# Performance work log

Hardware: AMD Instinct MI355X
Metric: run time of the kernel (lower is better)

## Reference

```python
import jax, jax.numpy as jnp
import numpy as np

EPS = 1e-05
IN_FEATURES = 1024
OUT_FEATURES = 512
M = 65536


def setup_inputs() -> dict:
    key = jax.random.key(0)
    k_x, k_w, k_b = jax.random.split(key, 3)
    x = jax.random.normal(k_x, (M, IN_FEATURES), dtype=jnp.float32)
    # kaiming_uniform(a=sqrt(5)) on [out, in]: bound = sqrt(6/((1+a^2)*fan_in)) = 1/sqrt(fan_in)
    bound = 1.0 / np.sqrt(IN_FEATURES)
    weight = jax.random.uniform(k_w, (OUT_FEATURES, IN_FEATURES), dtype=jnp.float32,
                                minval=-bound, maxval=bound)
    bias = jax.random.uniform(k_b, (OUT_FEATURES,), dtype=jnp.float32,
                              minval=-bound, maxval=bound)
    gamma = jnp.ones((OUT_FEATURES,), dtype=jnp.float32)
    beta = jnp.zeros((OUT_FEATURES,), dtype=jnp.float32)
    scale = jnp.ones((1,), dtype=jnp.float32)
    return {"x": x, "weight": weight, "bias": bias,
            "gamma": gamma, "beta": beta, "scale": scale}


def reference(x, weight, bias, gamma, beta, scale):
    # GEMM + bias: [M, N]
    acc = jnp.einsum('mk,nk->mn', x, weight) + bias[None, :]
    # Row-wise normalization over N (as the fused kernel computes per row)
    mean = jnp.mean(acc, axis=1, keepdims=True)
    var = jnp.mean((acc - mean) ** 2, axis=1, keepdims=True)
    normalized = (acc - mean) / jnp.sqrt(var + EPS)
    scaled = (normalized * gamma[None, :] + beta[None, :]) * scale[0]
    # Row softmax over N
    return jax.nn.softmax(scaled, axis=1)
```

## Files before the change

### kernel.cpp

```cpp
#include <hip/hip_runtime.h>
#include <hip/hip_bf16.h>

constexpr int KD = 1024;
constexpr int ND = 512;
constexpr int NT = 16;
constexpr float EPSV = 1e-5f;

using f32x4  = __attribute__((ext_vector_type(4))) float;
using bf16x8 = __attribute__((ext_vector_type(8))) short;
using u16x8  = __attribute__((ext_vector_type(8))) unsigned short;

__device__ __forceinline__ unsigned short f2bf(float f) {
  unsigned int u = __builtin_bit_cast(unsigned int, f);
  return (unsigned short)((u + 0x7fffu + ((u >> 16) & 1u)) >> 16);
}

__device__ __forceinline__ u16x8 pack8(float4 a, float4 b) {
  u16x8 v;
  v[0] = f2bf(a.x); v[1] = f2bf(a.y); v[2] = f2bf(a.z); v[3] = f2bf(a.w);
  v[4] = f2bf(b.x); v[5] = f2bf(b.y); v[6] = f2bf(b.z); v[7] = f2bf(b.w);
  return v;
}

__device__ __forceinline__ unsigned short cvt1(float f) {
  __hip_bfloat16 h = __float2bfloat16(f);
  return __builtin_bit_cast(unsigned short, h);
}

__device__ __forceinline__ void gload16(const void* g, void* l) {
  __builtin_amdgcn_global_load_lds(
      (const __attribute__((address_space(1))) void*)g,
      (__attribute__((address_space(3))) void*)l, 16, 0, 0);
}

#define WAITV4()  asm volatile("s_waitcnt vmcnt(4)" ::: "memory")
#define WAITV0()  asm volatile("s_waitcnt vmcnt(0)" ::: "memory")
#define LGKM0()   do { asm volatile("s_waitcnt lgkmcnt(0)" ::: "memory"); \
                       __builtin_amdgcn_sched_barrier(0); } while (0)
#define SCHEDB()  __builtin_amdgcn_sched_barrier(0)

__global__ void wconvert_kernel(const float* __restrict__ w,
                                unsigned short* __restrict__ wb) {
  int i = (blockIdx.x * blockDim.x + threadIdx.x) * 8;
  float4 a = *reinterpret_cast<const float4*>(w + i);
  float4 b = *reinterpret_cast<const float4*>(w + i + 4);
  *reinterpret_cast<u16x8*>(wb + i) = pack8(a, b);
}

__global__ __launch_bounds__(1024, 4)
void fused_kernel(const float* __restrict__ x,
                  const unsigned short* __restrict__ wb,
                  const float* __restrict__ bias,
                  const float* __restrict__ gamma,
                  const float* __restrict__ beta,
                  const float* __restrict__ scalep,
                  float* __restrict__ out) {
  __shared__ unsigned short As[2][128 * 64];
  __shared__ unsigned short Bs[2][512 * 64];

  const int tid  = threadIdx.x;
  const int lane = tid & 63;
  const int wid  = tid >> 6;
  const int wr   = wid >> 3;
  const int wcn  = wid & 7;
  const int l15  = lane & 15;
  const int lg   = lane >> 4;

  const long bm  = (long)blockIdx.x * 128;

  f32x4 acc[4][4] = {};

  const int arow0 = wid * 8 + lg;
  const float* asrc = x + (bm + arow0) * KD + l15 * 4;
  int aw[2];
  #pragma unroll
  for (int q = 0; q < 2; ++q) {
    int row = arow0 + q * 4;
    aw[q] = row * 128 + (((l15 >> 1) ^ (row & 7)) * 16) + ((l15 & 1) * 8);
  }

  int bsrc[4];
  #pragma unroll
  for (int p = 0; p < 4; ++p) {
    int n = p * 128 + (tid >> 3);
    int u = (tid & 7) ^ (n & 7);
    bsrc[p] = n * KD + u * 8;
  }

  int ard[4], brd[4];
  #pragma unroll
  for (int i = 0; i < 4; ++i) {
    int row = wr * 64 + i * 16 + l15;
    ard[i] = row * 128 + (lg ^ (row & 7)) * 16;
  }
  #pragma unroll
  for (int i = 0; i < 4; ++i) {
    int n = wcn * 64 + i * 16 + l15;
    brd[i] = n * 128 + (lg ^ (n & 7)) * 16;
  }

#define ISSUE_A(t) do { \
    qa0 = *reinterpret_cast<const float4*>(asrc + (t) * 64 + 0 * 4 * KD); \
    qa1 = *reinterpret_cast<const float4*>(asrc + (t) * 64 + 1 * 4 * KD); } while (0)

#define ISSUE_B(t, bufi) do { \
    gload16(wb + bsrc[0] + (t) * 64, (char*)Bs[bufi] + 0 * 16384 + tid * 16); \
    gload16(wb + bsrc[1] + (t) * 64, (char*)Bs[bufi] + 1 * 16384 + tid * 16); \
    gload16(wb + bsrc[2] + (t) * 64, (char*)Bs[bufi] + 2 * 16384 + tid * 16); \
    gload16(wb + bsrc[3] + (t) * 64, (char*)Bs[bufi] + 3 * 16384 + tid * 16); } while (0)

#define WA1(qr, qi, bufi) do { \
    union { unsigned short s[4]; unsigned long long v; } c_; \
    c_.s[0] = cvt1(qr.x); c_.s[1] = cvt1(qr.y); \
    c_.s[2] = cvt1(qr.z); c_.s[3] = cvt1(qr.w); \
    *reinterpret_cast<unsigned long long*>((char*)As[bufi] + aw[qi]) = c_.v; } while (0)

#define WRITE_A(bufi) do { const int wb_ = (bufi); \
    WA1(qa0, 0, wb_); WA1(qa1, 1, wb_); } while (0)

#define PHASE(ks, bufc) do { \
    const char* ab_ = (const char*)As[bufc]; \
    const char* bb_ = (const char*)Bs[bufc]; \
    const int kx_ = (ks) * 64; \
    bf16x8 b0_ = *reinterpret_cast<const bf16x8*>(bb_ + (brd[0] ^ kx_)); \
    bf16x8 b1_ = *reinterpret_cast<const bf16x8*>(bb_ + (brd[1] ^ kx_)); \
    bf16x8 b2_ = *reinterpret_cast<const bf16x8*>(bb_ + (brd[2] ^ kx_)); \
    bf16x8 b3_ = *reinterpret_cast<const bf16x8*>(bb_ + (brd[3] ^ kx_)); \
    bf16x8 a0_ = *reinterpret_cast<const bf16x8*>(ab_ + (ard[0] ^ kx_)); \
    bf16x8 a1_ = *reinterpret_cast<const bf16x8*>(ab_ + (ard[1] ^ kx_)); \
    bf16x8 a2_ = *reinterpret_cast<const bf16x8*>(ab_ + (ard[2] ^ kx_)); \
    bf16x8 a3_ = *reinterpret_cast<const bf16x8*>(ab_ + (ard[3] ^ kx_)); \
    LGKM0(); \
    __builtin_amdgcn_s_setprio(1); \
    acc[0][0] = __builtin_amdgcn_mfma_f32_16x16x32_bf16(a0_, b0_, acc[0][0], 0, 0, 0); \
    acc[0][1] = __builtin_amdgcn_mfma_f32_16x16x32_bf16(a0_, b1_, acc[0][1], 0, 0, 0); \
    acc[0][2] = __builtin_amdgcn_mfma_f32_16x16x32_bf16(a0_, b2_, acc[0][2], 0, 0, 0); \
    acc[0][3] = __builtin_amdgcn_mfma_f32_16x16x32_bf16(a0_, b3_, acc[0][3], 0, 0, 0); \
    acc[1][0] = __builtin_amdgcn_mfma_f32_16x16x32_bf16(a1_, b0_, acc[1][0], 0, 0, 0); \
    acc[1][1] = __builtin_amdgcn_mfma_f32_16x16x32_bf16(a1_, b1_, acc[1][1], 0, 0, 0); \
    acc[1][2] = __builtin_amdgcn_mfma_f32_16x16x32_bf16(a1_, b2_, acc[1][2], 0, 0, 0); \
    acc[1][3] = __builtin_amdgcn_mfma_f32_16x16x32_bf16(a1_, b3_, acc[1][3], 0, 0, 0); \
    acc[2][0] = __builtin_amdgcn_mfma_f32_16x16x32_bf16(a2_, b0_, acc[2][0], 0, 0, 0); \
    acc[2][1] = __builtin_amdgcn_mfma_f32_16x16x32_bf16(a2_, b1_, acc[2][1], 0, 0, 0); \
    acc[2][2] = __builtin_amdgcn_mfma_f32_16x16x32_bf16(a2_, b2_, acc[2][2], 0, 0, 0); \
    acc[2][3] = __builtin_amdgcn_mfma_f32_16x16x32_bf16(a2_, b3_, acc[2][3], 0, 0, 0); \
    acc[3][0] = __builtin_amdgcn_mfma_f32_16x16x32_bf16(a3_, b0_, acc[3][0], 0, 0, 0); \
    acc[3][1] = __builtin_amdgcn_mfma_f32_16x16x32_bf16(a3_, b1_, acc[3][1], 0, 0, 0); \
    acc[3][2] = __builtin_amdgcn_mfma_f32_16x16x32_bf16(a3_, b2_, acc[3][2], 0, 0, 0); \
    acc[3][3] = __builtin_amdgcn_mfma_f32_16x16x32_bf16(a3_, b3_, acc[3][3], 0, 0, 0); \
    __builtin_amdgcn_s_setprio(0); \
    SCHEDB(); } while (0)

  float4 qa0, qa1;

  ISSUE_A(0);    SCHEDB();
  ISSUE_B(0, 0); SCHEDB();
  WAITV4();
  WRITE_A(0);
  WAITV0();
  LGKM0();
  __builtin_amdgcn_s_barrier();
  SCHEDB();

  for (int t = 0; t < NT; ++t) {
    const int cur = t & 1;
    const int tp  = (t + 1 < NT) ? t + 1 : NT - 1;
    ISSUE_A(tp);          SCHEDB();
    ISSUE_B(tp, cur ^ 1); SCHEDB();
    PHASE(0, cur);
    PHASE(1, cur);
    WAITV4();
    WRITE_A(cur ^ 1);
    WAITV0();
    LGKM0();
    __builtin_amdgcn_s_barrier();
    SCHEDB();
  }

  float* redS = (float*)As[0];
  float* redQ = redS + 1152;
  float* rowA = redQ + 1152;
  float* rowB = rowA + 128;

  const int col0 = wcn * 64 + l15;
  const float sc = scalep[0];
  float bs4[4], gs4[4], bb4[4];
  #pragma unroll
  for (int ni = 0; ni < 4; ++ni) {
    bs4[ni] = bias[col0 + ni * 16];
    gs4[ni] = gamma[col0 + ni * 16] * sc;
    bb4[ni] = beta[col0 + ni * 16] * sc;
  }

  #pragma unroll
  for (int mi = 0; mi < 4; ++mi) {
    #pragma unroll
    for (int j = 0; j < 4; ++j) {
      float s = 0.f, q = 0.f;
      #pragma unroll
      for (int ni = 0; ni < 4; ++ni) {
        float v = acc[mi][ni][j] + bs4[ni];
        acc[mi][ni][j] = v;
        s += v;
        q = fmaf(v, v, q);
      }
      #pragma unroll
      for (int m = 1; m < 16; m <<= 1) {
        s += __shfl_xor(s, m, 64);
        q += __shfl_xor(q, m, 64);
      }
      if (l15 == 0) {
        int r = wr * 64 + mi * 16 + lg * 4 + j;
        redS[r * 9 + wcn] = s;
        redQ[r * 9 + wcn] = q;
      }
    }
  }
  __syncthreads();
  if (tid < 128) {
    float s = 0.f, q = 0.f;
    #pragma unroll
    for (int k = 0; k < 8; ++k) { s += redS[tid * 9 + k]; q += redQ[tid * 9 + k]; }
    float mu = s * (1.f / ND);
    rowA[tid] = mu;
    rowB[tid] = rsqrtf(q * (1.f / ND) - mu * mu + EPSV);
  }
  __syncthreads();

  #pragma unroll
  for (int mi = 0; mi < 4; ++mi) {
    #pragma unroll
    for (int j = 0; j < 4; ++j) {
      int r = wr * 64 + mi * 16 + lg * 4 + j;
      float mu = rowA[r], rs = rowB[r];
      float pm = -3.402823466e38f;
      #pragma unroll
      for (int ni = 0; ni < 4; ++ni) {
        float v = (acc[mi][ni][j] - mu) * rs;
        v = fmaf(v, gs4[ni], bb4[ni]);
        acc[mi][ni][j] = v;
        pm = fmaxf(pm, v);
      }
      #pragma unroll
      for (int m = 1; m < 16; m <<= 1) pm = fmaxf(pm, __shfl_xor(pm, m, 64));
      if (l15 == 0) redS[r * 9 + wcn] = pm;
    }
  }
  __syncthreads();
  if (tid < 128) {
    float m0 = fmaxf(fmaxf(redS[tid * 9 + 0], redS[tid * 9 + 1]),
                     fmaxf(redS[tid * 9 + 2], redS[tid * 9 + 3]));
    float m1 = fmaxf(fmaxf(redS[tid * 9 + 4], redS[tid * 9 + 5]),
                     fmaxf(redS[tid * 9 + 6], redS[tid * 9 + 7]));
    rowA[tid] = fmaxf(m0, m1);
  }
  __syncthreads();

  #pragma unroll
  for (int mi = 0; mi < 4; ++mi) {
    #pragma unroll
    for (int j = 0; j < 4; ++j) {
      int r = wr * 64 + mi * 16 + lg * 4 + j;
      float rmx = rowA[r];
      float ps = 0.f;
      #pragma unroll
      for (int ni = 0; ni < 4; ++ni) {
        float e = __expf(acc[mi][ni][j] - rmx);
        acc[mi][ni][j] = e;
        ps += e;
      }
      #pragma unroll
      for (int m = 1; m < 16; m <<= 1) ps += __shfl_xor(ps, m, 64);
      if (l15 == 0) redQ[r * 9 + wcn] = ps;
    }
  }
  __syncthreads();
  if (tid < 128) {
    float s = 0.f;
    #pragma unroll
    for (int k = 0; k < 8; ++k) s += redQ[tid * 9 + k];
    rowB[tid] = 1.f / s;
  }
  __syncthreads();

  #pragma unroll
  for (int mi = 0; mi < 4; ++mi) {
    #pragma unroll
    for (int j = 0; j < 4; ++j) {
      int r = wr * 64 + mi * 16 + lg * 4 + j;
      float rd = rowB[r];
      float* op = out + (bm + r) * ND + col0;
      #pragma unroll
      for (int ni = 0; ni < 4; ++ni)
        __builtin_nontemporal_store(acc[mi][ni][j] * rd, op + ni * 16);
    }
  }
#undef ISSUE_A
#undef ISSUE_B
#undef WA1
#undef WRITE_A
#undef PHASE
}

__global__ void fused_fallback(const float* __restrict__ x,
                               const float* __restrict__ wf,
                               const float* __restrict__ bias,
                               const float* __restrict__ gamma,
                               const float* __restrict__ beta,
                               const float* __restrict__ scalep,
                               float* __restrict__ out) {
  long row = blockIdx.x;
  int t = threadIdx.x;
  float s = 0.f;
  const float* xr = x + row * KD;
  const float* wr_ = wf + (size_t)t * KD;
  for (int k = 0; k < KD; ++k) s += xr[k] * wr_[k];
  s += bias[t];
  __shared__ float buf[ND];
  buf[t] = s;
  __syncthreads();
  __shared__ float red[2];
  if (t == 0) {
    float sum = 0.f, sq = 0.f;
    for (int i = 0; i < ND; ++i) { sum += buf[i]; sq += buf[i] * buf[i]; }
    float mu = sum / ND;
    red[0] = mu;
    red[1] = rsqrtf(sq / ND - mu * mu + EPSV);
  }
  __syncthreads();
  float zv = (s - red[0]) * red[1] * gamma[t] * scalep[0] + beta[t] * scalep[0];
  buf[t] = zv;
  __syncthreads();
  __shared__ float red2[2];
  if (t == 0) {
    float mxv = -3.4e38f;
    for (int i = 0; i < ND; ++i) mxv = fmaxf(mxv, buf[i]);
    float den = 0.f;
    for (int i = 0; i < ND; ++i) den += __expf(buf[i] - mxv);
    red2[0] = mxv; red2[1] = 1.f / den;
  }
  __syncthreads();
  out[row * ND + t] = __expf(zv - red2[0]) * red2[1];
}

extern "C" void kernel_launch(void* const* d_in, const int* in_sizes, int n_in,
                              void* d_out, int out_size, void* d_ws, size_t ws_size,
                              hipStream_t stream) {
  const float* x     = (const float*)d_in[0];
  const float* w     = (const float*)d_in[1];
  const float* bias  = (const float*)d_in[2];
  const float* gamma = (const float*)d_in[3];
  const float* beta  = (const float*)d_in[4];
  const float* scale = (const float*)d_in[5];
  float* out = (float*)d_out;

  const int Mrows = in_sizes[0] / KD;
  const size_t wb_bytes = (size_t)ND * KD * sizeof(unsigned short);

  if (ws_size >= wb_bytes) {
    unsigned short* wbuf = (unsigned short*)d_ws;
    wconvert_kernel<<<(ND * KD) / (256 * 8), 256, 0, stream>>>(w, wbuf);
    fused_kernel<<<Mrows / 128, 1024, 0, stream>>>(x, wbuf, bias, gamma, beta,
                                                   scale, out);
  } else {
    fused_fallback<<<Mrows, ND, 0, stream>>>(x, w, bias, gamma, beta, scale, out);
  }
}
```

Before: 139.1 us.

## Pre-swizzle weights into MFMA fragment layout and load B directly to registers

The weight conversion kernel now writes bf16 weights in a per-wave MFMA fragment order, so the GEMM loads its B operands straight from global memory (L2-resident) into registers instead of staging them through LDS. The block shrinks to 64 rows and 512 threads, with each of the 8 waves owning 64 output columns, and the K step goes from 64 to 32 with register double-buffering of B and LDS double-buffering of A. This removes the large B LDS buffers and the LDS read traffic and waits for B. In exchange each block re-reads the full weight matrix from global or L2, and the finer K step doubles the number of barriers.

```diff
diff --git a/kernel.cpp b/kernel.cpp
--- a/kernel.cpp
+++ b/kernel.cpp
@@ -3,7 +3,7 @@
 
 constexpr int KD = 1024;
 constexpr int ND = 512;
-constexpr int NT = 16;
+constexpr int NT = 32;
 constexpr float EPSV = 1e-5f;
 
 using f32x4  = __attribute__((ext_vector_type(4))) float;
@@ -27,27 +27,23 @@
   return __builtin_bit_cast(unsigned short, h);
 }
 
-__device__ __forceinline__ void gload16(const void* g, void* l) {
-  __builtin_amdgcn_global_load_lds(
-      (const __attribute__((address_space(1))) void*)g,
-      (__attribute__((address_space(3))) void*)l, 16, 0, 0);
-}
-
-#define WAITV4()  asm volatile("s_waitcnt vmcnt(4)" ::: "memory")
-#define WAITV0()  asm volatile("s_waitcnt vmcnt(0)" ::: "memory")
-#define LGKM0()   do { asm volatile("s_waitcnt lgkmcnt(0)" ::: "memory"); \
-                       __builtin_amdgcn_sched_barrier(0); } while (0)
 #define SCHEDB()  __builtin_amdgcn_sched_barrier(0)
 
 __global__ void wconvert_kernel(const float* __restrict__ w,
                                 unsigned short* __restrict__ wb) {
-  int i = (blockIdx.x * blockDim.x + threadIdx.x) * 8;
-  float4 a = *reinterpret_cast<const float4*>(w + i);
-  float4 b = *reinterpret_cast<const float4*>(w + i + 4);
-  *reinterpret_cast<u16x8*>(wb + i) = pack8(a, b);
-}
-
-__global__ __launch_bounds__(1024, 4)
+  int uid = blockIdx.x * blockDim.x + threadIdx.x;
+  int s   = uid >> 11;
+  int nf  = (uid >> 6) & 31;
+  int l   = uid & 63;
+  int n   = nf * 16 + (l & 15);
+  int k0  = s * 32 + (l >> 4) * 8;
+  const float* src = w + n * KD + k0;
+  float4 a = *reinterpret_cast<const float4*>(src);
+  float4 b = *reinterpret_cast<const float4*>(src + 4);
+  *reinterpret_cast<u16x8*>(wb + (size_t)uid * 8) = pack8(a, b);
+}
+
+__global__ __launch_bounds__(512, 4)
 void fused_kernel(const float* __restrict__ x,
                   const unsigned short* __restrict__ wb,
                   const float* __restrict__ bias,
@@ -55,134 +51,101 @@
                   const float* __restrict__ beta,
                   const float* __restrict__ scalep,
                   float* __restrict__ out) {
-  __shared__ unsigned short As[2][128 * 64];
-  __shared__ unsigned short Bs[2][512 * 64];
+  __shared__ unsigned short As[2][64 * 32];
 
   const int tid  = threadIdx.x;
   const int lane = tid & 63;
   const int wid  = tid >> 6;
-  const int wr   = wid >> 3;
-  const int wcn  = wid & 7;
   const int l15  = lane & 15;
   const int lg   = lane >> 4;
 
-  const long bm  = (long)blockIdx.x * 128;
+  const long bm  = (long)blockIdx.x * 64;
 
   f32x4 acc[4][4] = {};
 
-  const int arow0 = wid * 8 + lg;
-  const float* asrc = x + (bm + arow0) * KD + l15 * 4;
-  int aw[2];
-  #pragma unroll
-  for (int q = 0; q < 2; ++q) {
-    int row = arow0 + q * 4;
-    aw[q] = row * 128 + (((l15 >> 1) ^ (row & 7)) * 16) + ((l15 & 1) * 8);
-  }
-
-  int bsrc[4];
-  #pragma unroll
-  for (int p = 0; p < 4; ++p) {
-    int n = p * 128 + (tid >> 3);
-    int u = (tid & 7) ^ (n & 7);
-    bsrc[p] = n * KD + u * 8;
-  }
-
-  int ard[4], brd[4];
-  #pragma unroll
-  for (int i = 0; i < 4; ++i) {
-    int row = wr * 64 + i * 16 + l15;
-    ard[i] = row * 128 + (lg ^ (row & 7)) * 16;
-  }
-  #pragma unroll
-  for (int i = 0; i < 4; ++i) {
-    int n = wcn * 64 + i * 16 + l15;
-    brd[i] = n * 128 + (lg ^ (n & 7)) * 16;
-  }
-
-#define ISSUE_A(t) do { \
-    qa0 = *reinterpret_cast<const float4*>(asrc + (t) * 64 + 0 * 4 * KD); \
-    qa1 = *reinterpret_cast<const float4*>(asrc + (t) * 64 + 1 * 4 * KD); } while (0)
-
-#define ISSUE_B(t, bufi) do { \
-    gload16(wb + bsrc[0] + (t) * 64, (char*)Bs[bufi] + 0 * 16384 + tid * 16); \
-    gload16(wb + bsrc[1] + (t) * 64, (char*)Bs[bufi] + 1 * 16384 + tid * 16); \
-    gload16(wb + bsrc[2] + (t) * 64, (char*)Bs[bufi] + 2 * 16384 + tid * 16); \
-    gload16(wb + bsrc[3] + (t) * 64, (char*)Bs[bufi] + 3 * 16384 + tid * 16); } while (0)
-
-#define WA1(qr, qi, bufi) do { \
+  const int arow = tid >> 3;
+  const int akq  = tid & 7;
+  const float* asrc = x + (bm + arow) * KD + akq * 4;
+  const int awb = arow * 64 + (((akq >> 1) ^ ((arow >> 1) & 3)) * 16)
+                + ((akq & 1) * 8);
+
+  const int swa = (lg ^ ((l15 >> 1) & 3)) * 16;
+  int ard[4];
+  #pragma unroll
+  for (int mi = 0; mi < 4; ++mi) ard[mi] = (mi * 16 + l15) * 64 + swa;
+
+  const unsigned short* bbase = wb + ((size_t)(wid * 4) * 64 + lane) * 8;
+
+#define LOADA(t) (*reinterpret_cast<const float4*>(asrc + (t) * 32))
+
+#define LOADB(t, r0, r1, r2, r3) do { \
+    const unsigned short* bp_ = bbase + (t) * 16384; \
+    r0 = *reinterpret_cast<const bf16x8*>(bp_ + 0 * 512); \
+    r1 = *reinterpret_cast<const bf16x8*>(bp_ + 1 * 512); \
+    r2 = *reinterpret_cast<const bf16x8*>(bp_ + 2 * 512); \
+    r3 = *reinterpret_cast<const bf16x8*>(bp_ + 3 * 512); } while (0)
+
+#define WRITE_A(bufi) do { \
     union { unsigned short s[4]; unsigned long long v; } c_; \
-    c_.s[0] = cvt1(qr.x); c_.s[1] = cvt1(qr.y); \
-    c_.s[2] = cvt1(qr.z); c_.s[3] = cvt1(qr.w); \
-    *reinterpret_cast<unsigned long long*>((char*)As[bufi] + aw[qi]) = c_.v; } while (0)
-
-#define WRITE_A(bufi) do { const int wb_ = (bufi); \
-    WA1(qa0, 0, wb_); WA1(qa1, 1, wb_); } while (0)
-
-#define PHASE(ks, bufc) do { \
-    const char* ab_ = (const char*)As[bufc]; \
-    const char* bb_ = (const char*)Bs[bufc]; \
-    const int kx_ = (ks) * 64; \
-    bf16x8 b0_ = *reinterpret_cast<const bf16x8*>(bb_ + (brd[0] ^ kx_)); \
-    bf16x8 b1_ = *reinterpret_cast<const bf16x8*>(bb_ + (brd[1] ^ kx_)); \
-    bf16x8 b2_ = *reinterpret_cast<const bf16x8*>(bb_ + (brd[2] ^ kx_)); \
-    bf16x8 b3_ = *reinterpret_cast<const bf16x8*>(bb_ + (brd[3] ^ kx_)); \
-    bf16x8 a0_ = *reinterpret_cast<const bf16x8*>(ab_ + (ard[0] ^ kx_)); \
-    bf16x8 a1_ = *reinterpret_cast<const bf16x8*>(ab_ + (ard[1] ^ kx_)); \
-    bf16x8 a2_ = *reinterpret_cast<const bf16x8*>(ab_ + (ard[2] ^ kx_)); \
-    bf16x8 a3_ = *reinterpret_cast<const bf16x8*>(ab_ + (ard[3] ^ kx_)); \
-    LGKM0(); \
-    __builtin_amdgcn_s_setprio(1); \
-    acc[0][0] = __builtin_amdgcn_mfma_f32_16x16x32_bf16(a0_, b0_, acc[0][0], 0, 0, 0); \
-    acc[0][1] = __builtin_amdgcn_mfma_f32_16x16x32_bf16(a0_, b1_, acc[0][1], 0, 0, 0); \
-    acc[0][2] = __builtin_amdgcn_mfma_f32_16x16x32_bf16(a0_, b2_, acc[0][2], 0, 0, 0); \
-    acc[0][3] = __builtin_amdgcn_mfma_f32_16x16x32_bf16(a0_, b3_, acc[0][3], 0, 0, 0); \
-    acc[1][0] = __builtin_amdgcn_mfma_f32_16x16x32_bf16(a1_, b0_, acc[1][0], 0, 0, 0); \
-    acc[1][1] = __builtin_amdgcn_mfma_f32_16x16x32_bf16(a1_, b1_, acc[1][1], 0, 0, 0); \
-    acc[1][2] = __builtin_amdgcn_mfma_f32_16x16x32_bf16(a1_, b2_, acc[1][2], 0, 0, 0); \
-    acc[1][3] = __builtin_amdgcn_mfma_f32_16x16x32_bf16(a1_, b3_, acc[1][3], 0, 0, 0); \
-    acc[2][0] = __builtin_amdgcn_mfma_f32_16x16x32_bf16(a2_, b0_, acc[2][0], 0, 0, 0); \
-    acc[2][1] = __builtin_amdgcn_mfma_f32_16x16x32_bf16(a2_, b1_, acc[2][1], 0, 0, 0); \
-    acc[2][2] = __builtin_amdgcn_mfma_f32_16x16x32_bf16(a2_, b2_, acc[2][2], 0, 0, 0); \
-    acc[2][3] = __builtin_amdgcn_mfma_f32_16x16x32_bf16(a2_, b3_, acc[2][3], 0, 0, 0); \
-    acc[3][0] = __builtin_amdgcn_mfma_f32_16x16x32_bf16(a3_, b0_, acc[3][0], 0, 0, 0); \
-    acc[3][1] = __builtin_amdgcn_mfma_f32_16x16x32_bf16(a3_, b1_, acc[3][1], 0, 0, 0); \
-    acc[3][2] = __builtin_amdgcn_mfma_f32_16x16x32_bf16(a3_, b2_, acc[3][2], 0, 0, 0); \
-    acc[3][3] = __builtin_amdgcn_mfma_f32_16x16x32_bf16(a3_, b3_, acc[3][3], 0, 0, 0); \
-    __builtin_amdgcn_s_setprio(0); \
-    SCHEDB(); } while (0)
-
-  float4 qa0, qa1;
-
-  ISSUE_A(0);    SCHEDB();
-  ISSUE_B(0, 0); SCHEDB();
-  WAITV4();
+    c_.s[0] = cvt1(qa.x); c_.s[1] = cvt1(qa.y); \
+    c_.s[2] = cvt1(qa.z); c_.s[3] = cvt1(qa.w); \
+    *reinterpret_cast<unsigned long long*>((char*)As[bufi] + awb) = c_.v; } while (0)
+
+#define COMPUTE(bufi, B0, B1, B2, B3) do { \
+    const char* ab_ = (const char*)As[bufi]; \
+    bf16x8 a0_ = *reinterpret_cast<const bf16x8*>(ab_ + ard[0]); \
+    bf16x8 a1_ = *reinterpret_cast<const bf16x8*>(ab_ + ard[1]); \
+    bf16x8 a2_ = *reinterpret_cast<const bf16x8*>(ab_ + ard[2]); \
+    bf16x8 a3_ = *reinterpret_cast<const bf16x8*>(ab_ + ard[3]); \
+    acc[0][0] = __builtin_amdgcn_mfma_f32_16x16x32_bf16(a0_, B0, acc[0][0], 0, 0, 0); \
+    acc[0][1] = __builtin_amdgcn_mfma_f32_16x16x32_bf16(a0_, B1, acc[0][1], 0, 0, 0); \
+    acc[0][2] = __builtin_amdgcn_mfma_f32_16x16x32_bf16(a0_, B2, acc[0][2], 0, 0, 0); \
+    acc[0][3] = __builtin_amdgcn_mfma_f32_16x16x32_bf16(a0_, B3, acc[0][3], 0, 0, 0); \
+    acc[1][0] = __builtin_amdgcn_mfma_f32_16x16x32_bf16(a1_, B0, acc[1][0], 0, 0, 0); \
+    acc[1][1] = __builtin_amdgcn_mfma_f32_16x16x32_bf16(a1_, B1, acc[1][1], 0, 0, 0); \
+    acc[1][2] = __builtin_amdgcn_mfma_f32_16x16x32_bf16(a1_, B2, acc[1][2], 0, 0, 0); \
+    acc[1][3] = __builtin_amdgcn_mfma_f32_16x16x32_bf16(a1_, B3, acc[1][3], 0, 0, 0); \
+    acc[2][0] = __builtin_amdgcn_mfma_f32_16x16x32_bf16(a2_, B0, acc[2][0], 0, 0, 0); \
+    acc[2][1] = __builtin_amdgcn_mfma_f32_16x16x32_bf16(a2_, B1, acc[2][1], 0, 0, 0); \
+    acc[2][2] = __builtin_amdgcn_mfma_f32_16x16x32_bf16(a2_, B2, acc[2][2], 0, 0, 0); \
+    acc[2][3] = __builtin_amdgcn_mfma_f32_16x16x32_bf16(a2_, B3, acc[2][3], 0, 0, 0); \
+    acc[3][0] = __builtin_amdgcn_mfma_f32_16x16x32_bf16(a3_, B0, acc[3][0], 0, 0, 0); \
+    acc[3][1] = __builtin_amdgcn_mfma_f32_16x16x32_bf16(a3_, B1, acc[3][1], 0, 0, 0); \
+    acc[3][2] = __builtin_amdgcn_mfma_f32_16x16x32_bf16(a3_, B2, acc[3][2], 0, 0, 0); \
+    acc[3][3] = __builtin_amdgcn_mfma_f32_16x16x32_bf16(a3_, B3, acc[3][3], 0, 0, 0); \
+    } while (0)
+
+  float4 qa;
+  bf16x8 bc0, bc1, bc2, bc3, bn0, bn1, bn2, bn3;
+
+  qa = LOADA(0);
+  LOADB(0, bc0, bc1, bc2, bc3);
   WRITE_A(0);
-  WAITV0();
-  LGKM0();
-  __builtin_amdgcn_s_barrier();
-  SCHEDB();
-
-  for (int t = 0; t < NT; ++t) {
-    const int cur = t & 1;
-    const int tp  = (t + 1 < NT) ? t + 1 : NT - 1;
-    ISSUE_A(tp);          SCHEDB();
-    ISSUE_B(tp, cur ^ 1); SCHEDB();
-    PHASE(0, cur);
-    PHASE(1, cur);
-    WAITV4();
-    WRITE_A(cur ^ 1);
-    WAITV0();
-    LGKM0();
-    __builtin_amdgcn_s_barrier();
+  __syncthreads();
+
+  for (int t = 0; t < NT; t += 2) {
+    const int tp1 = (t + 1 < NT) ? t + 1 : NT - 1;
+    const int tp2 = (t + 2 < NT) ? t + 2 : NT - 1;
+    qa = LOADA(tp1);
+    LOADB(tp1, bn0, bn1, bn2, bn3);
     SCHEDB();
+    COMPUTE(0, bc0, bc1, bc2, bc3);
+    WRITE_A(1);
+    __syncthreads();
+    qa = LOADA(tp2);
+    LOADB(tp2, bc0, bc1, bc2, bc3);
+    SCHEDB();
+    COMPUTE(1, bn0, bn1, bn2, bn3);
+    WRITE_A(0);
+    __syncthreads();
   }
 
   float* redS = (float*)As[0];
-  float* redQ = redS + 1152;
-  float* rowA = redQ + 1152;
-  float* rowB = rowA + 128;
-
-  const int col0 = wcn * 64 + l15;
+  float* redQ = redS + 576;
+  float* rowA = redQ + 576;
+  float* rowB = rowA + 64;
+
+  const int col0 = wid * 64 + l15;
   const float sc = scalep[0];
   float bs4[4], gs4[4], bb4[4];
   #pragma unroll
@@ -210,14 +173,14 @@
         q += __shfl_xor(q, m, 64);
       }
       if (l15 == 0) {
-        int r = wr * 64 + mi * 16 + lg * 4 + j;
-        redS[r * 9 + wcn] = s;
-        redQ[r * 9 + wcn] = q;
+        int r = mi * 16 + lg * 4 + j;
+        redS[r * 9 + wid] = s;
+        redQ[r * 9 + wid] = q;
       }
     }
   }
   __syncthreads();
-  if (tid < 128) {
+  if (tid < 64) {
     float s = 0.f, q = 0.f;
     #pragma unroll
     for (int k = 0; k < 8; ++k) { s += redS[tid * 9 + k]; q += redQ[tid * 9 + k]; }
@@ -231,7 +194,7 @@
   for (int mi = 0; mi < 4; ++mi) {
     #pragma unroll
     for (int j = 0; j < 4; ++j) {
-      int r = wr * 64 + mi * 16 + lg * 4 + j;
+      int r = mi * 16 + lg * 4 + j;
       float mu = rowA[r], rs = rowB[r];
       float pm = -3.402823466e38f;
       #pragma unroll
@@ -243,11 +206,11 @@
       }
       #pragma unroll
       for (int m = 1; m < 16; m <<= 1) pm = fmaxf(pm, __shfl_xor(pm, m, 64));
-      if (l15 == 0) redS[r * 9 + wcn] = pm;
+      if (l15 == 0) redS[r * 9 + wid] = pm;
     }
   }
   __syncthreads();
-  if (tid < 128) {
+  if (tid < 64) {
     float m0 = fmaxf(fmaxf(redS[tid * 9 + 0], redS[tid * 9 + 1]),
                      fmaxf(redS[tid * 9 + 2], redS[tid * 9 + 3]));
     float m1 = fmaxf(fmaxf(redS[tid * 9 + 4], redS[tid * 9 + 5]),
@@ -260,7 +223,7 @@
   for (int mi = 0; mi < 4; ++mi) {
     #pragma unroll
     for (int j = 0; j < 4; ++j) {
-      int r = wr * 64 + mi * 16 + lg * 4 + j;
+      int r = mi * 16 + lg * 4 + j;
       float rmx = rowA[r];
       float ps = 0.f;
       #pragma unroll
@@ -271,11 +234,11 @@
       }
       #pragma unroll
       for (int m = 1; m < 16; m <<= 1) ps += __shfl_xor(ps, m, 64);
-      if (l15 == 0) redQ[r * 9 + wcn] = ps;
+      if (l15 == 0) redQ[r * 9 + wid] = ps;
     }
   }
   __syncthreads();
-  if (tid < 128) {
+  if (tid < 64) {
     float s = 0.f;
     #pragma unroll
     for (int k = 0; k < 8; ++k) s += redQ[tid * 9 + k];
@@ -287,7 +250,7 @@
   for (int mi = 0; mi < 4; ++mi) {
     #pragma unroll
     for (int j = 0; j < 4; ++j) {
-      int r = wr * 64 + mi * 16 + lg * 4 + j;
+      int r = mi * 16 + lg * 4 + j;
       float rd = rowB[r];
       float* op = out + (bm + r) * ND + col0;
       #pragma unroll
@@ -295,11 +258,10 @@
         __builtin_nontemporal_store(acc[mi][ni][j] * rd, op + ni * 16);
     }
   }
-#undef ISSUE_A
-#undef ISSUE_B
-#undef WA1
+#undef LOADA
+#undef LOADB
 #undef WRITE_A
-#undef PHASE
+#undef COMPUTE
 }
 
 __global__ void fused_fallback(const float* __restrict__ x,
@@ -359,9 +321,9 @@
 
   if (ws_size >= wb_bytes) {
     unsigned short* wbuf = (unsigned short*)d_ws;
-    wconvert_kernel<<<(ND * KD) / (256 * 8), 256, 0, stream>>>(w, wbuf);
-    fused_kernel<<<Mrows / 128, 1024, 0, stream>>>(x, wbuf, bias, gamma, beta,
-                                                   scale, out);
+    wconvert_kernel<<<(ND * KD / 8) / 256, 256, 0, stream>>>(w, wbuf);
+    fused_kernel<<<Mrows / 64, 512, 0, stream>>>(x, wbuf, bias, gamma, beta,
+                                                 scale, out);
   } else {
     fused_fallback<<<Mrows, ND, 0, stream>>>(x, w, bias, gamma, beta, scale, out);
   }
```

New measurement: 130.2 us. 1.07x faster.
